# Performance work log

Hardware: AMD Instinct MI355X
Metric: run time of the kernel (lower is better)

Reference implementation:

```python
import jax, jax.numpy as jnp
import numpy as np

TAU = 2.0
V_TH = 1.0
V_RESET = 0.0
ALPHA = 2.0  # ATan surrogate alpha (spikingjelly default)

@jax.custom_vjp
def spike(x):
    # Heaviside forward, ATan surrogate backward
    return (x >= 0).astype(x.dtype)

def _spike_fwd(x):
    return spike(x), x

def _spike_bwd(x, g):
    pix = (jnp.pi / 2) * ALPHA * x
    return (g * (ALPHA / 2) / (1 + pix * pix),)

spike.defvjp(_spike_fwd, _spike_bwd)

def setup_inputs() -> dict:
    key = jax.random.key(0)
    k1, k2, k3 = jax.random.split(key, 3)
    T, B, I, H = 256, 128, 512, 512
    x = jax.random.normal(k1, (T, B, I), dtype=jnp.float32)
    W = jax.random.normal(k2, (H, I), dtype=jnp.float32) * (1.0 / np.sqrt(I))
    b = jax.random.normal(k3, (H,), dtype=jnp.float32) * 0.01
    return {"x": x, "W": W, "b": b}

def reference(x, W, b):
    # Linear projection over all timesteps at once: (T,B,I) @ (H,I)^T -> (T,B,H)
    h = jnp.einsum('tbi,hi->tbh', x, W) + b

    def step(v, ht):
        # LIFNode, decay_input=False, v_reset=0: charge, fire, hard reset
        v = v - (v - V_RESET) / TAU + ht
        s = spike(v - V_TH)
        s_d = jax.lax.stop_gradient(s)  # detach_reset=True
        v = v * (1.0 - s_d) + V_RESET * s_d
        return v, s

    v0 = jnp.zeros_like(h[0])
    _, spikes = jax.lax.scan(step, v0, h)
    # dropout_p=0 (inference) -> identity; no synapse filter
    return spikes
```

## Files before the change

kernel.cpp:

```cpp
#include <hip/hip_runtime.h>

#define T_STEPS 256
#define B_DIM   128
#define I_DIM   512
#define H_DIM   512
#define M_DIM   (T_STEPS * B_DIM)

#define BM 128
#define BN 128
#define BK 32
#define LDA (BM + 4)
#define LDB (BN + 4)

__global__ __launch_bounds__(256, 2) void gemm_bias_f32(
    const float* __restrict__ A,
    const float* __restrict__ Bw,
    const float* __restrict__ bias,
    float* __restrict__ C)
{
    __shared__ float As[BK][LDA];
    __shared__ float Bs[BK][LDB];

    const int tid = threadIdx.x;
    const int tx  = tid & 15;
    const int ty  = tid >> 4;
    const int m0  = blockIdx.y * BM;
    const int n0  = blockIdx.x * BN;

    float acc[8][8];
    #pragma unroll
    for (int i = 0; i < 8; i++)
        #pragma unroll
        for (int j = 0; j < 8; j++)
            acc[i][j] = 0.0f;

    const int lrow = tid >> 3;
    const int lk   = (tid & 7) * 4;

    const float* Aptr = A  + (size_t)(m0 + lrow) * I_DIM + lk;
    const float* Bptr = Bw + (size_t)(n0 + lrow) * I_DIM + lk;

    for (int k0 = 0; k0 < I_DIM; k0 += BK) {
        float4 av[4], bv[4];
        #pragma unroll
        for (int p = 0; p < 4; p++) {
            av[p] = *(const float4*)(Aptr + (size_t)(p * 32) * I_DIM + k0);
            bv[p] = *(const float4*)(Bptr + (size_t)(p * 32) * I_DIM + k0);
        }

        __syncthreads();

        #pragma unroll
        for (int p = 0; p < 4; p++) {
            const int r = lrow + p * 32;
            As[lk + 0][r] = av[p].x;
            As[lk + 1][r] = av[p].y;
            As[lk + 2][r] = av[p].z;
            As[lk + 3][r] = av[p].w;
            Bs[lk + 0][r] = bv[p].x;
            Bs[lk + 1][r] = bv[p].y;
            Bs[lk + 2][r] = bv[p].z;
            Bs[lk + 3][r] = bv[p].w;
        }

        __syncthreads();

        for (int k = 0; k < BK; k++) {
            float4 a0 = *(const float4*)&As[k][ty * 8];
            float4 a1 = *(const float4*)&As[k][ty * 8 + 4];
            float4 b0 = *(const float4*)&Bs[k][tx * 8];
            float4 b1 = *(const float4*)&Bs[k][tx * 8 + 4];
            float a[8] = {a0.x, a0.y, a0.z, a0.w, a1.x, a1.y, a1.z, a1.w};
            float b[8] = {b0.x, b0.y, b0.z, b0.w, b1.x, b1.y, b1.z, b1.w};
            #pragma unroll
            for (int i = 0; i < 8; i++)
                #pragma unroll
                for (int j = 0; j < 8; j++)
                    acc[i][j] = fmaf(a[i], b[j], acc[i][j]);
        }
    }

    float bcol[8];
    #pragma unroll
    for (int j = 0; j < 8; j++)
        bcol[j] = bias[n0 + tx * 8 + j];

    #pragma unroll
    for (int i = 0; i < 8; i++) {
        const int m = m0 + ty * 8 + i;
        float4 o0, o1;
        o0.x = acc[i][0] + bcol[0];
        o0.y = acc[i][1] + bcol[1];
        o0.z = acc[i][2] + bcol[2];
        o0.w = acc[i][3] + bcol[3];
        o1.x = acc[i][4] + bcol[4];
        o1.y = acc[i][5] + bcol[5];
        o1.z = acc[i][6] + bcol[6];
        o1.w = acc[i][7] + bcol[7];
        float* cp = C + (size_t)m * H_DIM + n0 + tx * 8;
        *(float4*)(cp)     = o0;
        *(float4*)(cp + 4) = o1;
    }
}

#define SCAN_UNROLL 16
__global__ __launch_bounds__(256) void lif_scan(
    const float* __restrict__ h,
    float* __restrict__ out)
{
    const int n   = B_DIM * H_DIM;
    const int idx = blockIdx.x * 256 + threadIdx.x;
    const float* hp = h + idx;
    float* op = out + idx;

    float v = 0.0f;
    for (int t0 = 0; t0 < T_STEPS; t0 += SCAN_UNROLL) {
        float hv[SCAN_UNROLL];
        #pragma unroll
        for (int i = 0; i < SCAN_UNROLL; i++)
            hv[i] = hp[(size_t)(t0 + i) * n];

        float s[SCAN_UNROLL];
        #pragma unroll
        for (int i = 0; i < SCAN_UNROLL; i++) {
            v = 0.5f * v + hv[i];
            const bool fire = (v >= 1.0f);
            s[i] = fire ? 1.0f : 0.0f;
            v    = fire ? 0.0f : v;
        }

        #pragma unroll
        for (int i = 0; i < SCAN_UNROLL; i++)
            op[(size_t)(t0 + i) * n] = s[i];
    }
}

extern "C" void kernel_launch(void* const* d_in, const int* in_sizes, int n_in,
                              void* d_out, int out_size, void* d_ws, size_t ws_size,
                              hipStream_t stream) {
    const float* x = (const float*)d_in[0];
    const float* W = (const float*)d_in[1];
    const float* b = (const float*)d_in[2];
    float* out = (float*)d_out;
    float* h   = (float*)d_ws;

    dim3 grid(H_DIM / BN, M_DIM / BM);
    gemm_bias_f32<<<grid, 256, 0, stream>>>(x, W, b, h);

    lif_scan<<<(B_DIM * H_DIM) / 256, 256, 0, stream>>>(h, out);
}
```

Baseline: 306.8 us.

## Use k-contiguous smem layout in GEMM and double-buffer LIF scan loads

The GEMM now stores A and B tiles row-major along K with a padded stride, so smem stores become single float4 writes instead of transposed scalar scatters. Each thread now owns rows and columns strided by 16, and the inner loop reads float4 K-slices. The output store changes from float4 to strided scalar writes. The LIF scan software-pipelines its loads across two register buffers and uses nontemporal stores for the spikes. The launch-bounds occupancy hint is dropped, which may change register allocation.

Result: slower. 392.5 us (+27.9%).

```diff
diff --git a/kernel.cpp b/kernel.cpp
--- a/kernel.cpp
+++ b/kernel.cpp
@@ -9,17 +9,16 @@
 #define BM 128
 #define BN 128
 #define BK 32
-#define LDA (BM + 4)
-#define LDB (BN + 4)
+#define LDK 36
 
-__global__ __launch_bounds__(256, 2) void gemm_bias_f32(
+__global__ __launch_bounds__(256) void gemm_bias_f32(
     const float* __restrict__ A,
     const float* __restrict__ Bw,
     const float* __restrict__ bias,
     float* __restrict__ C)
 {
-    __shared__ float As[BK][LDA];
-    __shared__ float Bs[BK][LDB];
+    __shared__ float As[BM][LDK];
+    __shared__ float Bs[BN][LDK];
 
     const int tid = threadIdx.x;
     const int tx  = tid & 15;
@@ -52,58 +51,51 @@
 
         #pragma unroll
         for (int p = 0; p < 4; p++) {
-            const int r = lrow + p * 32;
-            As[lk + 0][r] = av[p].x;
-            As[lk + 1][r] = av[p].y;
-            As[lk + 2][r] = av[p].z;
-            As[lk + 3][r] = av[p].w;
-            Bs[lk + 0][r] = bv[p].x;
-            Bs[lk + 1][r] = bv[p].y;
-            Bs[lk + 2][r] = bv[p].z;
-            Bs[lk + 3][r] = bv[p].w;
+            *(float4*)&As[lrow + 32 * p][lk] = av[p];
+            *(float4*)&Bs[lrow + 32 * p][lk] = bv[p];
         }
 
         __syncthreads();
 
-        for (int k = 0; k < BK; k++) {
-            float4 a0 = *(const float4*)&As[k][ty * 8];
-            float4 a1 = *(const float4*)&As[k][ty * 8 + 4];
-            float4 b0 = *(const float4*)&Bs[k][tx * 8];
-            float4 b1 = *(const float4*)&Bs[k][tx * 8 + 4];
-            float a[8] = {a0.x, a0.y, a0.z, a0.w, a1.x, a1.y, a1.z, a1.w};
-            float b[8] = {b0.x, b0.y, b0.z, b0.w, b1.x, b1.y, b1.z, b1.w};
+        #pragma unroll
+        for (int k = 0; k < BK; k += 4) {
+            float4 af[8], bf[8];
+            #pragma unroll
+            for (int i = 0; i < 8; i++)
+                af[i] = *(const float4*)&As[ty + 16 * i][k];
+            #pragma unroll
+            for (int j = 0; j < 8; j++)
+                bf[j] = *(const float4*)&Bs[tx + 16 * j][k];
+
             #pragma unroll
             for (int i = 0; i < 8; i++)
                 #pragma unroll
-                for (int j = 0; j < 8; j++)
-                    acc[i][j] = fmaf(a[i], b[j], acc[i][j]);
+                for (int j = 0; j < 8; j++) {
+                    acc[i][j] = fmaf(af[i].x, bf[j].x, acc[i][j]);
+                    acc[i][j] = fmaf(af[i].y, bf[j].y, acc[i][j]);
+                    acc[i][j] = fmaf(af[i].z, bf[j].z, acc[i][j]);
+                    acc[i][j] = fmaf(af[i].w, bf[j].w, acc[i][j]);
+                }
         }
     }
 
     float bcol[8];
     #pragma unroll
     for (int j = 0; j < 8; j++)
-        bcol[j] = bias[n0 + tx * 8 + j];
+        bcol[j] = bias[n0 + tx + 16 * j];
 
     #pragma unroll
     for (int i = 0; i < 8; i++) {
-        const int m = m0 + ty * 8 + i;
-        float4 o0, o1;
-        o0.x = acc[i][0] + bcol[0];
-        o0.y = acc[i][1] + bcol[1];
-        o0.z = acc[i][2] + bcol[2];
-        o0.w = acc[i][3] + bcol[3];
-        o1.x = acc[i][4] + bcol[4];
-        o1.y = acc[i][5] + bcol[5];
-        o1.z = acc[i][6] + bcol[6];
-        o1.w = acc[i][7] + bcol[7];
-        float* cp = C + (size_t)m * H_DIM + n0 + tx * 8;
-        *(float4*)(cp)     = o0;
-        *(float4*)(cp + 4) = o1;
+        const int m = m0 + ty + 16 * i;
+        float* cp = C + (size_t)m * H_DIM + n0 + tx;
+        #pragma unroll
+        for (int j = 0; j < 8; j++)
+            cp[16 * j] = acc[i][j] + bcol[j];
     }
 }
 
-#define SCAN_UNROLL 16
+#define U 16
+#define NC (T_STEPS / U)
 __global__ __launch_bounds__(256) void lif_scan(
     const float* __restrict__ h,
     float* __restrict__ out)
@@ -113,25 +105,39 @@
     const float* hp = h + idx;
     float* op = out + idx;
 
+    float va[U], vb[U];
+    #pragma unroll
+    for (int i = 0; i < U; i++)
+        va[i] = hp[(size_t)i * n];
+
     float v = 0.0f;
-    for (int t0 = 0; t0 < T_STEPS; t0 += SCAN_UNROLL) {
-        float hv[SCAN_UNROLL];
+    for (int c = 0; c < NC; c += 2) {
+        if (c + 1 < NC) {
+            #pragma unroll
+            for (int i = 0; i < U; i++)
+                vb[i] = hp[(size_t)((c + 1) * U + i) * n];
+        }
         #pragma unroll
-        for (int i = 0; i < SCAN_UNROLL; i++)
-            hv[i] = hp[(size_t)(t0 + i) * n];
-
-        float s[SCAN_UNROLL];
+        for (int i = 0; i < U; i++) {
+            v = 0.5f * v + va[i];
+            const bool fire = (v >= 1.0f);
+            __builtin_nontemporal_store(fire ? 1.0f : 0.0f,
+                                        &op[(size_t)(c * U + i) * n]);
+            v = fire ? 0.0f : v;
+        }
+        if (c + 2 < NC) {
+            #pragma unroll
+            for (int i = 0; i < U; i++)
+                va[i] = hp[(size_t)((c + 2) * U + i) * n];
+        }
         #pragma unroll
-        for (int i = 0; i < SCAN_UNROLL; i++) {
-            v = 0.5f * v + hv[i];
+        for (int i = 0; i < U; i++) {
+            v = 0.5f * v + vb[i];
             const bool fire = (v >= 1.0f);
-            s[i] = fire ? 1.0f : 0.0f;
-            v    = fire ? 0.0f : v;
+            __builtin_nontemporal_store(fire ? 1.0f : 0.0f,
+                                        &op[(size_t)((c + 1) * U + i) * n]);
+            v = fire ? 0.0f : v;
         }
-
-        #pragma unroll
-        for (int i = 0; i < SCAN_UNROLL; i++)
-            op[(size_t)(t0 + i) * n] = s[i];
     }
 }
 
```
